# Kernel optimization log

Measured on AMD Instinct MI355X. Metric: run time of the kernel, lower is better.

## Reference

```python
import jax, jax.numpy as jnp
import numpy as np
import math

EMBED_DIM = 1024
NUM_HEADS = 16
HEAD_DIM = EMBED_DIM // NUM_HEADS
BATCH = 2
SEQ = 2048


def alibi_slopes(num_heads):
    def pow2_slopes(n):
        start = 2.0 ** (-(2.0 ** (-(math.log2(n) - 3))))
        return [start * (start ** i) for i in range(n)]
    if math.log2(num_heads).is_integer():
        s = pow2_slopes(num_heads)
    else:
        closest = 2 ** math.floor(math.log2(num_heads))
        s = pow2_slopes(closest)
        s += s[-1:] * (num_heads - closest)
    return jnp.asarray(s, dtype=jnp.float32)  # [H]


def setup_inputs() -> dict:
    key = jax.random.key(0)
    k1, k2, k3, k4, k5 = jax.random.split(key, 5)
    x = jax.random.normal(k1, (BATCH, SEQ, EMBED_DIM), dtype=jnp.float32)
    sd = 1.0 / math.sqrt(EMBED_DIM)
    Wqkv = jax.random.uniform(k2, (EMBED_DIM, 3 * EMBED_DIM), minval=-sd, maxval=sd, dtype=jnp.float32)
    bqkv = jax.random.uniform(k3, (3 * EMBED_DIM,), minval=-sd, maxval=sd, dtype=jnp.float32)
    Wout = jax.random.uniform(k4, (EMBED_DIM, EMBED_DIM), minval=-sd, maxval=sd, dtype=jnp.float32)
    bout = jax.random.uniform(k5, (EMBED_DIM,), minval=-sd, maxval=sd, dtype=jnp.float32)
    return {"x": x, "Wqkv": Wqkv, "bqkv": bqkv, "Wout": Wout, "bout": bout}


def reference(x, Wqkv, bqkv, Wout, bout):
    B, S, E = x.shape
    H, D = NUM_HEADS, HEAD_DIM
    qkv = x @ Wqkv + bqkv                       # [B,S,3E]
    qkv = qkv.reshape(B, S, H, 3 * D)
    q, k, v = jnp.split(qkv, 3, axis=-1)        # each [B,S,H,D]
    scores = jnp.einsum('bqhd,bkhd->bhqk', q, k) / math.sqrt(D)
    # ALiBi bias: distance[i,j] = j - i, scaled per-head
    pos = jnp.arange(S)
    distance = (pos[None, :] - pos[:, None]).astype(jnp.float32)  # [S,S]
    scores = scores + alibi_slopes(H)[None, :, None, None] * distance[None, None, :, :]
    attn = jax.nn.softmax(scores, axis=-1)      # [B,H,S,S]
    out = jnp.einsum('bhqk,bkhd->bqhd', attn, v).reshape(B, S, E)
    out = out @ Wout + bout
    return out, attn
```

## Files before the change

kernel.cpp:

```cpp
#include <hip/hip_runtime.h>

#define BATCH 2
#define SEQ   2048
#define EMB   1024
#define NH    16
#define HD    64

typedef __attribute__((ext_vector_type(8))) _Float16 half8;
typedef __attribute__((ext_vector_type(4))) _Float16 half4;
typedef __attribute__((ext_vector_type(4))) float floatx4;

#define LOG2E 1.44269504088896f
#define SCALE2 (0.125f * LOG2E)

#if __has_builtin(__builtin_amdgcn_exp2f)
__device__ __forceinline__ float fexp2(float x) { return __builtin_amdgcn_exp2f(x); }
#else
__device__ __forceinline__ float fexp2(float x) { return exp2f(x); }
#endif

__device__ __forceinline__ void lds_barrier() {
    asm volatile("s_waitcnt lgkmcnt(0)" ::: "memory");
    __builtin_amdgcn_s_barrier();
    __builtin_amdgcn_sched_barrier(0);
}

__global__ __launch_bounds__(256)
void cvt_f16(const float* __restrict__ in, _Float16* __restrict__ out, int n8) {
    int i = blockIdx.x * 256 + threadIdx.x;
    if (i >= n8) return;
    float4 a = ((const float4*)in)[2 * i];
    float4 b = ((const float4*)in)[2 * i + 1];
    half8 h = {(_Float16)a.x, (_Float16)a.y, (_Float16)a.z, (_Float16)a.w,
               (_Float16)b.x, (_Float16)b.y, (_Float16)b.z, (_Float16)b.w};
    ((half8*)out)[i] = h;
}

__global__ __launch_bounds__(256)
void transpose_both(const float* __restrict__ Wqkv, const float* __restrict__ Wout,
                    _Float16* __restrict__ Wh, _Float16* __restrict__ Oh) {
    __shared__ float t[32][33];
    const int K = EMB;
    const float* W; _Float16* o; int N, n0;
    if (blockIdx.x < 96) { W = Wqkv; o = Wh; N = 3 * EMB; n0 = blockIdx.x * 32; }
    else                 { W = Wout; o = Oh; N = EMB;     n0 = (blockIdx.x - 96) * 32; }
    const int k0 = blockIdx.y * 32;
    const int r = threadIdx.x >> 3, c4 = (threadIdx.x & 7) * 4;
    float4 v = *(const float4*)&W[(size_t)(k0 + r) * N + n0 + c4];
    t[r][c4 + 0] = v.x; t[r][c4 + 1] = v.y;
    t[r][c4 + 2] = v.z; t[r][c4 + 3] = v.w;
    __syncthreads();
    half4 hv;
#pragma unroll
    for (int j = 0; j < 4; ++j) hv[j] = (_Float16)t[c4 + j][r];
    *(half4*)&o[(size_t)(n0 + r) * K + k0 + c4] = hv;
}

#define ALD 40

__global__ __launch_bounds__(256)
void gemm_qkv_mfma(const _Float16* __restrict__ Xh, const _Float16* __restrict__ Wh,
                   const float* __restrict__ bias,
                   _Float16* __restrict__ Qh, _Float16* __restrict__ Kh,
                   _Float16* __restrict__ Vh) {
    const int K = EMB;
    __shared__ _Float16 Ah[2][128 * ALD];
    __shared__ _Float16 Bh[2][128 * ALD];

    const int tid  = threadIdx.x;
    const int wave = tid >> 6, lane = tid & 63;
    const int quad = lane >> 4, lp = lane & 15;

    const int linear = blockIdx.y * 24 + blockIdx.x;
    const int swz = (linear & 7) * 96 + (linear >> 3);
    const int bx = swz % 24, by = swz / 24;
    const int row0 = by * 128, col0 = bx * 128;
    const int wm = (wave >> 1) * 64, wn = (wave & 1) * 64;

    const int srow = tid >> 2, sseg = (tid & 3) * 8;

    floatx4 acc[4][4];
#pragma unroll
    for (int i = 0; i < 4; ++i)
#pragma unroll
        for (int j = 0; j < 4; ++j) acc[i][j] = (floatx4){0.f, 0.f, 0.f, 0.f};

    uint4 a0 = *(const uint4*)&Xh[(size_t)(row0 + srow) * K + sseg];
    uint4 a1 = *(const uint4*)&Xh[(size_t)(row0 + srow + 64) * K + sseg];
    uint4 b0 = *(const uint4*)&Wh[(size_t)(col0 + srow) * K + sseg];
    uint4 b1 = *(const uint4*)&Wh[(size_t)(col0 + srow + 64) * K + sseg];
    *(uint4*)&Ah[0][srow * ALD + sseg] = a0;
    *(uint4*)&Ah[0][(srow + 64) * ALD + sseg] = a1;
    *(uint4*)&Bh[0][srow * ALD + sseg] = b0;
    *(uint4*)&Bh[0][(srow + 64) * ALD + sseg] = b1;

    int cur = 0;
    for (int k0 = 0; k0 < K; k0 += 32) {
        __syncthreads();
        if (k0 + 32 < K) {
            a0 = *(const uint4*)&Xh[(size_t)(row0 + srow) * K + k0 + 32 + sseg];
            a1 = *(const uint4*)&Xh[(size_t)(row0 + srow + 64) * K + k0 + 32 + sseg];
            b0 = *(const uint4*)&Wh[(size_t)(col0 + srow) * K + k0 + 32 + sseg];
            b1 = *(const uint4*)&Wh[(size_t)(col0 + srow + 64) * K + k0 + 32 + sseg];
        }

        half8 ah[4];
#pragma unroll
        for (int mi = 0; mi < 4; ++mi)
            ah[mi] = *(const half8*)&Ah[cur][(wm + mi * 16 + lp) * ALD + quad * 8];
#pragma unroll
        for (int ni = 0; ni < 4; ++ni) {
            half8 bh = *(const half8*)&Bh[cur][(wn + ni * 16 + lp) * ALD + quad * 8];
#pragma unroll
            for (int mi = 0; mi < 4; ++mi)
                acc[mi][ni] = __builtin_amdgcn_mfma_f32_16x16x32_f16(
                    ah[mi], bh, acc[mi][ni], 0, 0, 0);
        }

        if (k0 + 32 < K) {
            *(uint4*)&Ah[cur ^ 1][srow * ALD + sseg] = a0;
            *(uint4*)&Ah[cur ^ 1][(srow + 64) * ALD + sseg] = a1;
            *(uint4*)&Bh[cur ^ 1][srow * ALD + sseg] = b0;
            *(uint4*)&Bh[cur ^ 1][(srow + 64) * ALD + sseg] = b1;
            cur ^= 1;
        }
    }

#pragma unroll
    for (int ni = 0; ni < 4; ++ni) {
        const int c = col0 + wn + ni * 16 + lp;
        const int h = c / 192;
        const int rem = c - h * 192;
        const int which = rem >> 6;
        const int d = rem & 63;
        _Float16* __restrict__ P = (which == 0) ? Qh : (which == 1) ? Kh : Vh;
        const float bb = bias[c];
        const float sc = (which == 0) ? SCALE2 : 1.0f;
#pragma unroll
        for (int mi = 0; mi < 4; ++mi) {
            floatx4 a = acc[mi][ni];
#pragma unroll
            for (int r = 0; r < 4; ++r) {
                int m = row0 + wm + mi * 16 + quad * 4 + r;
                int b = m >> 11, s = m & (SEQ - 1);
                P[((size_t)(b * NH + h) * SEQ + s) * HD + d] =
                    (_Float16)((a[r] + bb) * sc);
            }
        }
    }
}

__global__ __launch_bounds__(256)
void gemm_out_mfma(const _Float16* __restrict__ Ch, const _Float16* __restrict__ Oh,
                   const float* __restrict__ bias, float* __restrict__ out) {
    const int K = EMB, N = EMB;
    __shared__ _Float16 Ah[2][128 * ALD];
    __shared__ _Float16 Bh[2][128 * ALD];

    const int tid  = threadIdx.x;
    const int wave = tid >> 6, lane = tid & 63;
    const int quad = lane >> 4, lp = lane & 15;

    const int linear = blockIdx.y * 8 + blockIdx.x;
    const int swz = (linear & 7) * 32 + (linear >> 3);
    const int bx = swz & 7, by = swz >> 3;
    const int row0 = by * 128, col0 = bx * 128;
    const int wm = (wave >> 1) * 64, wn = (wave & 1) * 64;

    const int srow = tid >> 2, sseg = (tid & 3) * 8;

    floatx4 acc[4][4];
#pragma unroll
    for (int i = 0; i < 4; ++i)
#pragma unroll
        for (int j = 0; j < 4; ++j) acc[i][j] = (floatx4){0.f, 0.f, 0.f, 0.f};

    uint4 a0 = *(const uint4*)&Ch[(size_t)(row0 + srow) * K + sseg];
    uint4 a1 = *(const uint4*)&Ch[(size_t)(row0 + srow + 64) * K + sseg];
    uint4 b0 = *(const uint4*)&Oh[(size_t)(col0 + srow) * K + sseg];
    uint4 b1 = *(const uint4*)&Oh[(size_t)(col0 + srow + 64) * K + sseg];
    *(uint4*)&Ah[0][srow * ALD + sseg] = a0;
    *(uint4*)&Ah[0][(srow + 64) * ALD + sseg] = a1;
    *(uint4*)&Bh[0][srow * ALD + sseg] = b0;
    *(uint4*)&Bh[0][(srow + 64) * ALD + sseg] = b1;

    int cur = 0;
    for (int k0 = 0; k0 < K; k0 += 32) {
        __syncthreads();
        if (k0 + 32 < K) {
            a0 = *(const uint4*)&Ch[(size_t)(row0 + srow) * K + k0 + 32 + sseg];
            a1 = *(const uint4*)&Ch[(size_t)(row0 + srow + 64) * K + k0 + 32 + sseg];
            b0 = *(const uint4*)&Oh[(size_t)(col0 + srow) * K + k0 + 32 + sseg];
            b1 = *(const uint4*)&Oh[(size_t)(col0 + srow + 64) * K + k0 + 32 + sseg];
        }

        half8 ah[4];
#pragma unroll
        for (int mi = 0; mi < 4; ++mi)
            ah[mi] = *(const half8*)&Ah[cur][(wm + mi * 16 + lp) * ALD + quad * 8];
#pragma unroll
        for (int ni = 0; ni < 4; ++ni) {
            half8 bh = *(const half8*)&Bh[cur][(wn + ni * 16 + lp) * ALD + quad * 8];
#pragma unroll
            for (int mi = 0; mi < 4; ++mi)
                acc[mi][ni] = __builtin_amdgcn_mfma_f32_16x16x32_f16(
                    ah[mi], bh, acc[mi][ni], 0, 0, 0);
        }

        if (k0 + 32 < K) {
            *(uint4*)&Ah[cur ^ 1][srow * ALD + sseg] = a0;
            *(uint4*)&Ah[cur ^ 1][(srow + 64) * ALD + sseg] = a1;
            *(uint4*)&Bh[cur ^ 1][srow * ALD + sseg] = b0;
            *(uint4*)&Bh[cur ^ 1][(srow + 64) * ALD + sseg] = b1;
            cur ^= 1;
        }
    }

#pragma unroll
    for (int ni = 0; ni < 4; ++ni) {
        const int c = col0 + wn + ni * 16 + lp;
        const float bb = bias[c];
#pragma unroll
        for (int mi = 0; mi < 4; ++mi) {
            floatx4 a = acc[mi][ni];
#pragma unroll
            for (int r = 0; r < 4; ++r) {
                int m = row0 + wm + mi * 16 + quad * 4 + r;
                out[(size_t)m * N + c] = a[r] + bb;
            }
        }
    }
}

#define KT 64
#define LDST 72
#define NTILE (SEQ / KT)

__global__ __launch_bounds__(256)
void attn_stats(const _Float16* __restrict__ Qh,
                const _Float16* __restrict__ Kh,
                float* __restrict__ off2g) {
    __shared__ _Float16 ksb[2][KT * LDST];

    const int tid  = threadIdx.x;
    const int wave = tid >> 6, lane = tid & 63;
    const int quad = lane >> 4, lp = lane & 15;
    const int q0 = blockIdx.x * 64;
    const int bh = blockIdx.y;
    const int h  = bh & (NH - 1);
    const float slope2 = exp2f(-0.5f * (float)(h + 1)) * LOG2E;

    const _Float16* Qbase = Qh + ((size_t)bh * SEQ + q0) * HD;
    const _Float16* Kbase = Kh + (size_t)bh * SEQ * HD;

    const half8 qa0 = *(const half8*)&Qbase[(size_t)(16 * wave + lp) * HD + quad * 8];
    const half8 qa1 = *(const half8*)&Qbase[(size_t)(16 * wave + lp) * HD + 32 + quad * 8];

    const int qg = q0 + 16 * wave + lp;
    const float aq = -slope2 * (float)qg;

    const int srow0 = tid >> 3, srow1 = 32 + (tid >> 3), sseg = tid & 7;

    float m0 = -1e30f, mxv = -1e30f, lsum = 0.f;

    uint4 k0r = *(const uint4*)&Kbase[(size_t)srow0 * HD + sseg * 8];
    uint4 k1r = *(const uint4*)&Kbase[(size_t)srow1 * HD + sseg * 8];
    *(uint4*)&ksb[0][srow0 * LDST + sseg * 8] = k0r;
    *(uint4*)&ksb[0][srow1 * LDST + sseg * 8] = k1r;
    lds_barrier();

    int cur = 0;
    for (int kt = 0; kt < NTILE; ++kt) {
        if (kt) lds_barrier();
        if (kt + 1 < NTILE) {
            size_t goff = (size_t)(kt + 1) * KT * HD + sseg * 8;
            k0r = *(const uint4*)&Kbase[goff + (size_t)srow0 * HD];
            k1r = *(const uint4*)&Kbase[goff + (size_t)srow1 * HD];
        }
        const _Float16* ks = ksb[cur];

        floatx4 cc[4];
        __builtin_amdgcn_s_setprio(1);
#pragma unroll
        for (int t = 0; t < 4; ++t) {
            half8 b0 = *(const half8*)&ks[(16 * t + lp) * LDST + quad * 8];
            half8 b1 = *(const half8*)&ks[(16 * t + lp) * LDST + 32 + quad * 8];
            floatx4 c = {0.f, 0.f, 0.f, 0.f};
            c = __builtin_amdgcn_mfma_f32_16x16x32_f16(b0, qa0, c, 0, 0, 0);
            cc[t] = __builtin_amdgcn_mfma_f32_16x16x32_f16(b1, qa1, c, 0, 0, 0);
        }
        __builtin_amdgcn_s_setprio(0);
#pragma unroll
        for (int t = 0; t < 4; ++t) {
            float kb = (float)(kt * KT + 16 * t + 4 * quad);
            float s0 = cc[t][0] + fmaf(slope2, kb,       aq);
            float s1 = cc[t][1] + fmaf(slope2, kb + 1.f, aq);
            float s2 = cc[t][2] + fmaf(slope2, kb + 2.f, aq);
            float s3 = cc[t][3] + fmaf(slope2, kb + 3.f, aq);
            float tm = fmaxf(fmaxf(s0, s1), fmaxf(s2, s3));
            mxv = fmaxf(mxv, tm);
            if (mxv > m0 + 8.f) {
                lsum *= fexp2(m0 - mxv);
                m0 = mxv;
            }
            lsum += fexp2(s0 - m0) + fexp2(s1 - m0) +
                    fexp2(s2 - m0) + fexp2(s3 - m0);
        }

        if (kt + 1 < NTILE) {
            *(uint4*)&ksb[cur ^ 1][srow0 * LDST + sseg * 8] = k0r;
            *(uint4*)&ksb[cur ^ 1][srow1 * LDST + sseg * 8] = k1r;
            cur ^= 1;
        }
    }

    float mm = mxv;
    float ll = lsum * fexp2(m0 - mm);
#pragma unroll
    for (int off = 16; off < 64; off <<= 1) {
        float mo = __shfl_xor(mm, off);
        float lo = __shfl_xor(ll, off);
        float mn = fmaxf(mm, mo);
        ll = ll * fexp2(mm - mn) + lo * fexp2(mo - mn);
        mm = mn;
    }
    if (quad == 0)
        off2g[(size_t)bh * SEQ + qg] = mm + __log2f(ll);
}

#define QT 128

__global__ __launch_bounds__(512)
void attn_pv(const _Float16* __restrict__ Qh,
             const _Float16* __restrict__ Kh,
             const _Float16* __restrict__ Vh,
             const float* __restrict__ off2g,
             float* __restrict__ attn,
             _Float16* __restrict__ ctx) {
    __shared__ _Float16 ksb[2][KT * LDST];
    __shared__ _Float16 vtb[2][HD * LDST];
    __shared__ _Float16 ps[QT * LDST];

    const int tid  = threadIdx.x;
    const int wave = tid >> 6, lane = tid & 63;
    const int quad = lane >> 4, lp = lane & 15;
    const int q0 = blockIdx.x * QT;
    const int bh = blockIdx.y;
    const int h  = bh & (NH - 1);
    const float slope2 = exp2f(-0.5f * (float)(h + 1)) * LOG2E;

    const _Float16* Qbase = Qh + ((size_t)bh * SEQ + q0) * HD;
    const _Float16* Kbase = Kh + (size_t)bh * SEQ * HD;
    const _Float16* Vbase = Vh + (size_t)bh * SEQ * HD;

    const half8 qa0 = *(const half8*)&Qbase[(size_t)(16 * wave + lp) * HD + quad * 8];
    const half8 qa1 = *(const half8*)&Qbase[(size_t)(16 * wave + lp) * HD + 32 + quad * 8];

    const int qg = q0 + 16 * wave + lp;
    const float off2 = off2g[(size_t)bh * SEQ + qg];
    const float aq2 = -slope2 * (float)qg - off2;

    const int srow = tid >> 3, sseg = tid & 7;
    const int kvx = srow ^ (sseg << 3);

    floatx4 o[4];
#pragma unroll
    for (int t = 0; t < 4; ++t) o[t] = (floatx4){0.f, 0.f, 0.f, 0.f};

    float* arow = attn + (size_t)bh * SEQ * SEQ +
                  (size_t)(q0 + 16 * wave + lp) * SEQ + 4 * quad;

    uint4 kreg, vreg;
    kreg = *(const uint4*)&Kbase[(size_t)srow * HD + sseg * 8];
    vreg = *(const uint4*)&Vbase[(size_t)srow * HD + sseg * 8];
    *(uint4*)&ksb[0][srow * LDST + sseg * 8] = kreg;
    {
        union { uint4 u; _Float16 e[8]; } vv; vv.u = vreg;
#pragma unroll
        for (int j = 0; j < 8; ++j)
            vtb[0][(sseg * 8 + j) * LDST + kvx] = vv.e[j];
    }
    lds_barrier();

    int cur = 0;
    for (int kt = 0; kt < NTILE; ++kt) {
        if (kt) lds_barrier();
        if (kt + 1 < NTILE) {
            size_t goff = (size_t)(kt + 1) * KT * HD + (size_t)srow * HD + sseg * 8;
            kreg = *(const uint4*)&Kbase[goff];
            vreg = *(const uint4*)&Vbase[goff];
        }
        const _Float16* ks = ksb[cur];
        const _Float16* vt = vtb[cur];

        __builtin_amdgcn_s_setprio(1);
#pragma unroll
        for (int t = 0; t < 4; ++t) {
            half8 b0 = *(const half8*)&ks[(16 * t + lp) * LDST + quad * 8];
            half8 b1 = *(const half8*)&ks[(16 * t + lp) * LDST + 32 + quad * 8];
            floatx4 c = {0.f, 0.f, 0.f, 0.f};
            c = __builtin_amdgcn_mfma_f32_16x16x32_f16(b0, qa0, c, 0, 0, 0);
            c = __builtin_amdgcn_mfma_f32_16x16x32_f16(b1, qa1, c, 0, 0, 0);
            float kb = (float)(kt * KT + 16 * t + 4 * quad);
            float p0 = fexp2(c[0] + fmaf(slope2, kb,       aq2));
            float p1 = fexp2(c[1] + fmaf(slope2, kb + 1.f, aq2));
            float p2 = fexp2(c[2] + fmaf(slope2, kb + 2.f, aq2));
            float p3 = fexp2(c[3] + fmaf(slope2, kb + 3.f, aq2));
            float4 pw = {p0, p1, p2, p3};
            *(float4*)&arow[kt * KT + 16 * t] = pw;
            const int col = 16 * t + 4 * quad;
            half4 ph = {(_Float16)p0, (_Float16)p1, (_Float16)p2, (_Float16)p3};
            *(half4*)&ps[(16 * wave + lp) * LDST + col] = ph;
        }
        __builtin_amdgcn_s_setprio(0);

        half8 pa0 = *(const half8*)&ps[(16 * wave + lp) * LDST + quad * 8];
        half8 pa1 = *(const half8*)&ps[(16 * wave + lp) * LDST + 32 + quad * 8];
        __builtin_amdgcn_s_setprio(1);
#pragma unroll
        for (int t = 0; t < 4; ++t) {
            int g = 2 * t + (lp >> 3);
            half8 vb0 = *(const half8*)&vt[(16 * t + lp) * LDST + ((quad ^ g) << 3)];
            half8 vb1 = *(const half8*)&vt[(16 * t + lp) * LDST + (((quad + 4) ^ g) << 3)];
            o[t] = __builtin_amdgcn_mfma_f32_16x16x32_f16(pa0, vb0, o[t], 0, 0, 0);
            o[t] = __builtin_amdgcn_mfma_f32_16x16x32_f16(pa1, vb1, o[t], 0, 0, 0);
        }
        __builtin_amdgcn_s_setprio(0);

        if (kt + 1 < NTILE) {
            *(uint4*)&ksb[cur ^ 1][srow * LDST + sseg * 8] = kreg;
            union { uint4 u; _Float16 e[8]; } vv; vv.u = vreg;
#pragma unroll
            for (int j = 0; j < 8; ++j)
                vtb[cur ^ 1][(sseg * 8 + j) * LDST + kvx] = vv.e[j];
            cur ^= 1;
        }
    }

    const int b = bh >> 4;
#pragma unroll
    for (int t = 0; t < 4; ++t)
#pragma unroll
        for (int r = 0; r < 4; ++r)
            ctx[((size_t)(b * SEQ + q0 + 16 * wave + quad * 4 + r)) * EMB +
                h * HD + 16 * t + lp] = (_Float16)o[t][r];
}


extern "C" void kernel_launch(void* const* d_in, const int* in_sizes, int n_in,
                              void* d_out, int out_size, void* d_ws, size_t ws_size,
                              hipStream_t stream) {
    const float* x    = (const float*)d_in[0];
    const float* Wqkv = (const float*)d_in[1];
    const float* bqkv = (const float*)d_in[2];
    const float* Wout = (const float*)d_in[3];
    const float* bout = (const float*)d_in[4];

    float* out  = (float*)d_out;
    float* attn = out + (size_t)BATCH * SEQ * EMB;

    const size_t HE = (size_t)BATCH * NH * SEQ * HD;
    const size_t XE = (size_t)BATCH * SEQ * EMB;
    _Float16* Qh = (_Float16*)d_ws;
    _Float16* Kh = Qh + HE;
    _Float16* Vh = Kh + HE;
    _Float16* Ch = Vh + HE;
    _Float16* Xh = Ch + XE;
    _Float16* Wh = Xh + XE;
    _Float16* Oh = Wh + (size_t)3 * EMB * EMB;
    float* off2g = (float*)(Oh + (size_t)EMB * EMB);

    cvt_f16<<<dim3(2048), dim3(256), 0, stream>>>(x, Xh, (int)(XE / 8));
    transpose_both<<<dim3(128, 32), dim3(256), 0, stream>>>(Wqkv, Wout, Wh, Oh);

    gemm_qkv_mfma<<<dim3(24, 32), dim3(256), 0, stream>>>(
        Xh, Wh, bqkv, Qh, Kh, Vh);

    attn_stats<<<dim3(SEQ / 64, BATCH * NH), dim3(256), 0, stream>>>(
        Qh, Kh, off2g);

    attn_pv<<<dim3(SEQ / QT, BATCH * NH), dim3(512), 0, stream>>>(
        Qh, Kh, Vh, off2g, attn, Ch);

    gemm_out_mfma<<<dim3(8, 32), dim3(256), 0, stream>>>(Ch, Oh, bout, out);
}
```

Baseline: 258.7 us.

## Split attention PV over key halves and merge partial contexts

The attn_pv kernel now launches twice as many blocks, each covering half of the key tiles, and writes a partial context to one of two buffers. A new merge_ctx kernel adds the two partials before the output GEMM. K/V LDS double buffering is replaced by a single buffer with an extra barrier per tile, and launch bounds now request higher occupancy. The goal is more parallelism and occupancy on the attention stage, which is dominated by writing the probability matrix. The cost is an extra kernel, extra context traffic, and less load/compute overlap inside each block.

```diff
diff --git a/kernel.cpp b/kernel.cpp
--- a/kernel.cpp
+++ b/kernel.cpp
@@ -329,16 +329,18 @@
 }
 
 #define QT 128
-
-__global__ __launch_bounds__(512)
+#define NT2 (NTILE / 2)
+
+__global__ __launch_bounds__(512, 8)
 void attn_pv(const _Float16* __restrict__ Qh,
              const _Float16* __restrict__ Kh,
              const _Float16* __restrict__ Vh,
              const float* __restrict__ off2g,
              float* __restrict__ attn,
-             _Float16* __restrict__ ctx) {
-    __shared__ _Float16 ksb[2][KT * LDST];
-    __shared__ _Float16 vtb[2][HD * LDST];
+             _Float16* __restrict__ ctx0,
+             _Float16* __restrict__ ctx1) {
+    __shared__ _Float16 ks[KT * LDST];
+    __shared__ _Float16 vt[HD * LDST];
     __shared__ _Float16 ps[QT * LDST];
 
     const int tid  = threadIdx.x;
@@ -346,12 +348,14 @@
     const int quad = lane >> 4, lp = lane & 15;
     const int q0 = blockIdx.x * QT;
     const int bh = blockIdx.y;
+    const int kz = blockIdx.z;
     const int h  = bh & (NH - 1);
     const float slope2 = exp2f(-0.5f * (float)(h + 1)) * LOG2E;
 
     const _Float16* Qbase = Qh + ((size_t)bh * SEQ + q0) * HD;
     const _Float16* Kbase = Kh + (size_t)bh * SEQ * HD;
     const _Float16* Vbase = Vh + (size_t)bh * SEQ * HD;
+    _Float16* __restrict__ ctxp = kz ? ctx1 : ctx0;
 
     const half8 qa0 = *(const half8*)&Qbase[(size_t)(16 * wave + lp) * HD + quad * 8];
     const half8 qa1 = *(const half8*)&Qbase[(size_t)(16 * wave + lp) * HD + 32 + quad * 8];
@@ -370,28 +374,31 @@
     float* arow = attn + (size_t)bh * SEQ * SEQ +
                   (size_t)(q0 + 16 * wave + lp) * SEQ + 4 * quad;
 
+    const int kt0 = kz * NT2;
+
     uint4 kreg, vreg;
-    kreg = *(const uint4*)&Kbase[(size_t)srow * HD + sseg * 8];
-    vreg = *(const uint4*)&Vbase[(size_t)srow * HD + sseg * 8];
-    *(uint4*)&ksb[0][srow * LDST + sseg * 8] = kreg;
+    {
+        size_t goff = (size_t)kt0 * KT * HD + (size_t)srow * HD + sseg * 8;
+        kreg = *(const uint4*)&Kbase[goff];
+        vreg = *(const uint4*)&Vbase[goff];
+    }
+    *(uint4*)&ks[srow * LDST + sseg * 8] = kreg;
     {
         union { uint4 u; _Float16 e[8]; } vv; vv.u = vreg;
 #pragma unroll
         for (int j = 0; j < 8; ++j)
-            vtb[0][(sseg * 8 + j) * LDST + kvx] = vv.e[j];
+            vt[(sseg * 8 + j) * LDST + kvx] = vv.e[j];
     }
     lds_barrier();
 
-    int cur = 0;
-    for (int kt = 0; kt < NTILE; ++kt) {
-        if (kt) lds_barrier();
-        if (kt + 1 < NTILE) {
+    for (int kl = 0; kl < NT2; ++kl) {
+        const int kt = kt0 + kl;
+        if (kl) lds_barrier();
+        if (kl + 1 < NT2) {
             size_t goff = (size_t)(kt + 1) * KT * HD + (size_t)srow * HD + sseg * 8;
             kreg = *(const uint4*)&Kbase[goff];
             vreg = *(const uint4*)&Vbase[goff];
         }
-        const _Float16* ks = ksb[cur];
-        const _Float16* vt = vtb[cur];
 
         __builtin_amdgcn_s_setprio(1);
 #pragma unroll
@@ -427,13 +434,13 @@
         }
         __builtin_amdgcn_s_setprio(0);
 
-        if (kt + 1 < NTILE) {
-            *(uint4*)&ksb[cur ^ 1][srow * LDST + sseg * 8] = kreg;
+        lds_barrier();
+        if (kl + 1 < NT2) {
+            *(uint4*)&ks[srow * LDST + sseg * 8] = kreg;
             union { uint4 u; _Float16 e[8]; } vv; vv.u = vreg;
 #pragma unroll
             for (int j = 0; j < 8; ++j)
-                vtb[cur ^ 1][(sseg * 8 + j) * LDST + kvx] = vv.e[j];
-            cur ^= 1;
+                vt[(sseg * 8 + j) * LDST + kvx] = vv.e[j];
         }
     }
 
@@ -442,8 +449,20 @@
     for (int t = 0; t < 4; ++t)
 #pragma unroll
         for (int r = 0; r < 4; ++r)
-            ctx[((size_t)(b * SEQ + q0 + 16 * wave + quad * 4 + r)) * EMB +
-                h * HD + 16 * t + lp] = (_Float16)o[t][r];
+            ctxp[((size_t)(b * SEQ + q0 + 16 * wave + quad * 4 + r)) * EMB +
+                 h * HD + 16 * t + lp] = (_Float16)o[t][r];
+}
+
+__global__ __launch_bounds__(256)
+void merge_ctx(_Float16* __restrict__ a, const _Float16* __restrict__ b, int n8) {
+    int i = blockIdx.x * 256 + threadIdx.x;
+    if (i >= n8) return;
+    half8 x = ((const half8*)a)[i];
+    half8 y = ((const half8*)b)[i];
+    half8 z;
+#pragma unroll
+    for (int j = 0; j < 8; ++j) z[j] = (_Float16)((float)x[j] + (float)y[j]);
+    ((half8*)a)[i] = z;
 }
 
 
@@ -465,7 +484,8 @@
     _Float16* Kh = Qh + HE;
     _Float16* Vh = Kh + HE;
     _Float16* Ch = Vh + HE;
-    _Float16* Xh = Ch + XE;
+    _Float16* Cp = Ch + XE;
+    _Float16* Xh = Cp + XE;
     _Float16* Wh = Xh + XE;
     _Float16* Oh = Wh + (size_t)3 * EMB * EMB;
     float* off2g = (float*)(Oh + (size_t)EMB * EMB);
@@ -479,8 +499,11 @@
     attn_stats<<<dim3(SEQ / 64, BATCH * NH), dim3(256), 0, stream>>>(
         Qh, Kh, off2g);
 
-    attn_pv<<<dim3(SEQ / QT, BATCH * NH), dim3(512), 0, stream>>>(
-        Qh, Kh, Vh, off2g, attn, Ch);
+    attn_pv<<<dim3(SEQ / QT, BATCH * NH, 2), dim3(512), 0, stream>>>(
+        Qh, Kh, Vh, off2g, attn, Ch, Cp);
+
+    merge_ctx<<<dim3((unsigned)(XE / 8 / 256)), dim3(256), 0, stream>>>(
+        Ch, Cp, (int)(XE / 8));
 
     gemm_out_mfma<<<dim3(8, 32), dim3(256), 0, stream>>>(Ch, Oh, bout, out);
 }
```

Result: slower. 328.8 us (+27.1%).
